# Optimization experiments

Hardware: AMD Instinct MI355X
Metric: run time of the kernel (lower is better)

## Reference

```python
import jax, jax.numpy as jnp
import numpy as np

B, S, T = 64, 512, 256  # batch, seq_len, num_tags


def setup_inputs() -> dict:
    key = jax.random.key(0)
    k1, k2, k3, k4 = jax.random.split(key, 4)
    emissions = jax.random.normal(k1, (B, S, T), dtype=jnp.float32)
    tags = jax.random.randint(k2, (B, S), 0, T, dtype=jnp.int32)
    mask = jnp.ones((B, S), dtype=bool)
    # nn.init.uniform_(-0.01, 0.01) as in reset_parameters()
    transitions = jax.random.uniform(k3, (T, T), minval=-0.01, maxval=0.01, dtype=jnp.float32)
    tse = jax.random.uniform(k4, (T + 2, T + 2), minval=-0.01, maxval=0.01, dtype=jnp.float32)
    tse = tse.at[T + 1, T].set(-10000.0)  # transitions[end_tag, start_tag] = -10000
    return {"emissions": emissions, "tags": tags, "mask": mask,
            "transitions": transitions, "transitions_with_start_end": tse}


def reference(emissions, tags, mask, transitions, transitions_with_start_end):
    Bv, Sv, Tv = emissions.shape
    start, end = Tv, Tv + 1

    # ---- forward algorithm (log partition), faithful to the torch recurrence:
    # new[b, j] = alpha[b, j] + logsumexp_k( trans[k, j] + emit_t[b, k] )
    # (the mask line fv*mask + fv*~mask in the original is a no-op)
    alpha0 = emissions[:, 0] + transitions_with_start_end[start, :Tv]

    def step(alpha, em_t):  # em_t: [B, T]
        lse = jax.nn.logsumexp(transitions[None, :, :] + em_t[:, :, None], axis=1)  # [B, T]
        return alpha + lse, None

    ems = jnp.swapaxes(emissions[:, 1:], 0, 1)  # [S-1, B, T]
    alpha, _ = jax.lax.scan(step, alpha0, ems)
    forward_score = jax.nn.logsumexp(alpha + transitions_with_start_end[:Tv, end], axis=1)  # [B]

    # ---- gold path score
    mf = mask.astype(emissions.dtype)
    emit = jnp.take_along_axis(emissions, tags[:, :, None].astype(jnp.int32), axis=2)[:, :, 0]  # [B, S]
    score = transitions_with_start_end[start, tags[:, 0]]
    score = score + jnp.sum(emit * mf, axis=1)
    score = score + jnp.sum(transitions[tags[:, 1:], tags[:, :-1]] * mf[:, 1:], axis=1)
    last_idx = jnp.sum(mask.astype(jnp.int32), axis=1) - 1  # [B]
    last_tags = jnp.take_along_axis(tags, last_idx[:, None], axis=1)[:, 0]
    score = score + transitions_with_start_end[last_tags, end]

    return forward_score - score  # negative log-likelihood per batch element, [B]
```

## Files before the change

### kernel.cpp

```cpp
#include <hip/hip_runtime.h>
#include <cstdint>

#define B_ 64
#define S_ 512
#define T_ 256
#define TP2 258

#define BM 64
#define BK 32
#define LDA 40
#define LDB 40

typedef __attribute__((ext_vector_type(8))) short short8;
typedef __attribute__((ext_vector_type(4))) float f32x4;

__device__ __forceinline__ ushort f2bf(float f) {
    union { float f; uint32_t u; } c; c.f = f;
    uint32_t u = c.u;
    u += 0x7FFFu + ((u >> 16) & 1u);
    return (ushort)(u >> 16);
}

__global__ void prep_w(const float* __restrict__ trans, ushort* __restrict__ wt) {
    int n = blockIdx.x;
    int k = threadIdx.x;
    wt[n * T_ + k] = f2bf(__expf(trans[k * T_ + n]));
}

__global__ __launch_bounds__(256) void gemm_lse(
    const float* __restrict__ em, const ushort* __restrict__ wt,
    float* __restrict__ accb)
{
    __shared__ ushort Alds[BM * LDA];
    __shared__ ushort Blds[T_ * LDB];

    int blk  = blockIdx.x;
    long r0  = (long)blk * BM;
    int batch = (int)(r0 / S_);
    bool has_s0 = (r0 % S_) == 0;

    int tid  = threadIdx.x;
    int wave = tid >> 6;
    int lane = tid & 63;
    int quad = lane >> 4;
    int l15  = lane & 15;

    f32x4 acc[4][4];
    for (int i = 0; i < 4; ++i)
        for (int j = 0; j < 4; ++j)
            acc[i][j] = (f32x4){0.f, 0.f, 0.f, 0.f};

    int srow = tid >> 2;
    int skc  = (tid & 3) * 8;

    for (int kt = 0; kt < T_ / BK; ++kt) {
        int k0 = kt * BK;
        {
            const float* src = em + (r0 + srow) * T_ + k0 + skc;
            float4 va = *(const float4*)(src);
            float4 vb = *(const float4*)(src + 4);
            union { ushort u[8]; uint4 v; } pk;
            pk.u[0] = f2bf(__expf(va.x)); pk.u[1] = f2bf(__expf(va.y));
            pk.u[2] = f2bf(__expf(va.z)); pk.u[3] = f2bf(__expf(va.w));
            pk.u[4] = f2bf(__expf(vb.x)); pk.u[5] = f2bf(__expf(vb.y));
            pk.u[6] = f2bf(__expf(vb.z)); pk.u[7] = f2bf(__expf(vb.w));
            *(uint4*)&Alds[srow * LDA + skc] = pk.v;
        }
        for (int p = 0; p < 4; ++p) {
            int idx = tid + p * 256;
            int n   = idx >> 2;
            int kc  = (idx & 3) * 8;
            uint4 v = *(const uint4*)&wt[n * T_ + k0 + kc];
            *(uint4*)&Blds[n * LDB + kc] = v;
        }
        __syncthreads();

        short8 af[4], bf[4];
        for (int i = 0; i < 4; ++i)
            af[i] = *(const short8*)&Alds[(i * 16 + l15) * LDA + quad * 8];
        for (int j = 0; j < 4; ++j)
            bf[j] = *(const short8*)&Blds[(wave * 64 + j * 16 + l15) * LDB + quad * 8];
        for (int i = 0; i < 4; ++i)
            for (int j = 0; j < 4; ++j)
                acc[i][j] = __builtin_amdgcn_mfma_f32_16x16x32_bf16(af[i], bf[j], acc[i][j], 0, 0, 0);
        __syncthreads();
    }

    for (int j = 0; j < 4; ++j) {
        float s = 0.f;
        for (int i = 0; i < 4; ++i) {
            f32x4 a = acc[i][j];
            for (int v = 0; v < 4; ++v) {
                bool skip = has_s0 && (i == 0) && (quad == 0) && (v == 0);
                if (!skip) s += __logf(a[v]);
            }
        }
        s += __shfl_xor(s, 16);
        s += __shfl_xor(s, 32);
        if (lane < 16)
            atomicAdd(&accb[batch * T_ + wave * 64 + j * 16 + lane], s);
    }
}

__global__ __launch_bounds__(256) void finalize(
    const float* __restrict__ em, const int* __restrict__ tags,
    const float* __restrict__ trans, const float* __restrict__ tse,
    const float* __restrict__ accb, float* __restrict__ out)
{
    __shared__ float red[8];
    int b = blockIdx.x;
    int j = threadIdx.x;
    int w = j >> 6;

    float v = em[(long)b * S_ * T_ + j] + tse[T_ * TP2 + j]
            + accb[b * T_ + j] + tse[j * TP2 + (T_ + 1)];

    float m = v;
    for (int o = 32; o; o >>= 1) m = fmaxf(m, __shfl_xor(m, o));
    if ((j & 63) == 0) red[w] = m;
    __syncthreads();
    m = fmaxf(fmaxf(red[0], red[1]), fmaxf(red[2], red[3]));

    float e = __expf(v - m);
    for (int o = 32; o; o >>= 1) e += __shfl_xor(e, o);
    if ((j & 63) == 0) red[4 + w] = e;
    __syncthreads();
    float fwd = m + __logf(red[4] + red[5] + red[6] + red[7]);

    const int* tg = tags + b * S_;
    float sc = 0.f;
    for (int s = j; s < S_; s += 256) {
        int t = tg[s];
        sc += em[((long)b * S_ + s) * T_ + t];
        if (s >= 1) sc += trans[t * T_ + tg[s - 1]];
    }
    if (j == 0) {
        sc += tse[T_ * TP2 + tg[0]];
        sc += tse[tg[S_ - 1] * TP2 + (T_ + 1)];
    }
    for (int o = 32; o; o >>= 1) sc += __shfl_xor(sc, o);
    __syncthreads();
    if ((j & 63) == 0) red[w] = sc;
    __syncthreads();
    if (j == 0) out[b] = fwd - (red[0] + red[1] + red[2] + red[3]);
}

extern "C" void kernel_launch(void* const* d_in, const int* in_sizes, int n_in,
                              void* d_out, int out_size, void* d_ws, size_t ws_size,
                              hipStream_t stream) {
    const float* em    = (const float*)d_in[0];
    const int*   tags  = (const int*)d_in[1];
    const float* trans = (const float*)d_in[3];
    const float* tse   = (const float*)d_in[4];
    float* out = (float*)d_out;

    ushort* wt   = (ushort*)d_ws;
    float*  accb = (float*)((char*)d_ws + 131072);

    hipMemsetAsync(accb, 0, B_ * T_ * sizeof(float), stream);
    prep_w<<<T_, T_, 0, stream>>>(trans, wt);
    gemm_lse<<<(B_ * S_) / BM, 256, 0, stream>>>(em, wt, accb);
    finalize<<<B_, T_, 0, stream>>>(em, tags, trans, tse, accb, out);
}
```

Measured before the change: 96.73 us.

## Prefetch GEMM tiles into registers, replace atomics with partials, move gold score into GEMM

The GEMM kernel now loads the next K-tile of emissions and exp-weights into registers while the MFMAs of the current tile run, hiding global-load latency. Atomic accumulation is replaced by per-block partial sums that finalize adds up, so the memset launch goes away. The gold-path score is computed inside the GEMM blocks, one row per lane, instead of a serial loop in finalize. This costs more registers, which may lower occupancy, and adds workspace for the partials.

```diff
diff --git a/kernel.cpp b/kernel.cpp
--- a/kernel.cpp
+++ b/kernel.cpp
@@ -29,15 +29,18 @@
 
 __global__ __launch_bounds__(256) void gemm_lse(
     const float* __restrict__ em, const ushort* __restrict__ wt,
-    float* __restrict__ accb)
+    const int* __restrict__ tags, const float* __restrict__ trans,
+    const float* __restrict__ tse,
+    float* __restrict__ accP, float* __restrict__ scoreP)
 {
     __shared__ ushort Alds[BM * LDA];
     __shared__ ushort Blds[T_ * LDB];
 
-    int blk  = blockIdx.x;
-    long r0  = (long)blk * BM;
-    int batch = (int)(r0 / S_);
-    bool has_s0 = (r0 % S_) == 0;
+    int blk   = blockIdx.x;
+    long r0   = (long)blk * BM;
+    int batch = blk >> 3;
+    int s0    = (blk & 7) * BM;
+    bool has_s0 = (s0 == 0);
 
     int tid  = threadIdx.x;
     int wave = tid >> 6;
@@ -53,12 +56,18 @@
     int srow = tid >> 2;
     int skc  = (tid & 3) * 8;
 
+    const float* aptr = em + (r0 + srow) * T_ + skc;
+    float4 va = *(const float4*)(aptr);
+    float4 vb = *(const float4*)(aptr + 4);
+    uint4 bv[4];
+    #pragma unroll
+    for (int p = 0; p < 4; ++p) {
+        int idx = tid + p * 256;
+        bv[p] = *(const uint4*)&wt[(idx >> 2) * T_ + (idx & 3) * 8];
+    }
+
     for (int kt = 0; kt < T_ / BK; ++kt) {
-        int k0 = kt * BK;
         {
-            const float* src = em + (r0 + srow) * T_ + k0 + skc;
-            float4 va = *(const float4*)(src);
-            float4 vb = *(const float4*)(src + 4);
             union { ushort u[8]; uint4 v; } pk;
             pk.u[0] = f2bf(__expf(va.x)); pk.u[1] = f2bf(__expf(va.y));
             pk.u[2] = f2bf(__expf(va.z)); pk.u[3] = f2bf(__expf(va.w));
@@ -66,30 +75,46 @@
             pk.u[6] = f2bf(__expf(vb.z)); pk.u[7] = f2bf(__expf(vb.w));
             *(uint4*)&Alds[srow * LDA + skc] = pk.v;
         }
+        #pragma unroll
         for (int p = 0; p < 4; ++p) {
             int idx = tid + p * 256;
-            int n   = idx >> 2;
-            int kc  = (idx & 3) * 8;
-            uint4 v = *(const uint4*)&wt[n * T_ + k0 + kc];
-            *(uint4*)&Blds[n * LDB + kc] = v;
+            *(uint4*)&Blds[(idx >> 2) * LDB + (idx & 3) * 8] = bv[p];
         }
         __syncthreads();
 
+        if (kt < T_ / BK - 1) {
+            int k1 = (kt + 1) * BK;
+            va = *(const float4*)(aptr + k1);
+            vb = *(const float4*)(aptr + k1 + 4);
+            #pragma unroll
+            for (int p = 0; p < 4; ++p) {
+                int idx = tid + p * 256;
+                bv[p] = *(const uint4*)&wt[(idx >> 2) * T_ + k1 + (idx & 3) * 8];
+            }
+        }
+
         short8 af[4], bf[4];
+        #pragma unroll
         for (int i = 0; i < 4; ++i)
             af[i] = *(const short8*)&Alds[(i * 16 + l15) * LDA + quad * 8];
+        #pragma unroll
         for (int j = 0; j < 4; ++j)
             bf[j] = *(const short8*)&Blds[(wave * 64 + j * 16 + l15) * LDB + quad * 8];
+        #pragma unroll
         for (int i = 0; i < 4; ++i)
+            #pragma unroll
             for (int j = 0; j < 4; ++j)
                 acc[i][j] = __builtin_amdgcn_mfma_f32_16x16x32_bf16(af[i], bf[j], acc[i][j], 0, 0, 0);
         __syncthreads();
     }
 
+    #pragma unroll
     for (int j = 0; j < 4; ++j) {
         float s = 0.f;
+        #pragma unroll
         for (int i = 0; i < 4; ++i) {
             f32x4 a = acc[i][j];
+            #pragma unroll
             for (int v = 0; v < 4; ++v) {
                 bool skip = has_s0 && (i == 0) && (quad == 0) && (v == 0);
                 if (!skip) s += __logf(a[v]);
@@ -98,51 +123,63 @@
         s += __shfl_xor(s, 16);
         s += __shfl_xor(s, 32);
         if (lane < 16)
-            atomicAdd(&accb[batch * T_ + wave * 64 + j * 16 + lane], s);
+            accP[blk * T_ + wave * 64 + j * 16 + lane] = s;
+    }
+
+    {
+        float sc = 0.f;
+        if (lane < 16) {
+            int sl = s0 + wave * 16 + lane;
+            const int* tg = tags + batch * S_;
+            int t = tg[sl];
+            sc = em[((long)batch * S_ + sl) * T_ + t];
+            if (sl >= 1) sc += trans[t * T_ + tg[sl - 1]];
+            else         sc += tse[T_ * TP2 + t];
+            if (sl == S_ - 1) sc += tse[t * TP2 + (T_ + 1)];
+        }
+        #pragma unroll
+        for (int o = 32; o; o >>= 1) sc += __shfl_xor(sc, o);
+        if (lane == 0) scoreP[blk * 4 + wave] = sc;
     }
 }
 
 __global__ __launch_bounds__(256) void finalize(
-    const float* __restrict__ em, const int* __restrict__ tags,
-    const float* __restrict__ trans, const float* __restrict__ tse,
-    const float* __restrict__ accb, float* __restrict__ out)
+    const float* __restrict__ em, const float* __restrict__ tse,
+    const float* __restrict__ accP, const float* __restrict__ scoreP,
+    float* __restrict__ out)
 {
     __shared__ float red[8];
     int b = blockIdx.x;
     int j = threadIdx.x;
     int w = j >> 6;
 
+    float p = 0.f;
+    #pragma unroll
+    for (int q = 0; q < 8; ++q)
+        p += accP[((b << 3) + q) * T_ + j];
+
     float v = em[(long)b * S_ * T_ + j] + tse[T_ * TP2 + j]
-            + accb[b * T_ + j] + tse[j * TP2 + (T_ + 1)];
+            + p + tse[j * TP2 + (T_ + 1)];
 
     float m = v;
+    #pragma unroll
     for (int o = 32; o; o >>= 1) m = fmaxf(m, __shfl_xor(m, o));
     if ((j & 63) == 0) red[w] = m;
     __syncthreads();
     m = fmaxf(fmaxf(red[0], red[1]), fmaxf(red[2], red[3]));
 
     float e = __expf(v - m);
+    #pragma unroll
     for (int o = 32; o; o >>= 1) e += __shfl_xor(e, o);
     if ((j & 63) == 0) red[4 + w] = e;
     __syncthreads();
     float fwd = m + __logf(red[4] + red[5] + red[6] + red[7]);
 
-    const int* tg = tags + b * S_;
-    float sc = 0.f;
-    for (int s = j; s < S_; s += 256) {
-        int t = tg[s];
-        sc += em[((long)b * S_ + s) * T_ + t];
-        if (s >= 1) sc += trans[t * T_ + tg[s - 1]];
-    }
-    if (j == 0) {
-        sc += tse[T_ * TP2 + tg[0]];
-        sc += tse[tg[S_ - 1] * TP2 + (T_ + 1)];
-    }
-    for (int o = 32; o; o >>= 1) sc += __shfl_xor(sc, o);
-    __syncthreads();
-    if ((j & 63) == 0) red[w] = sc;
-    __syncthreads();
-    if (j == 0) out[b] = fwd - (red[0] + red[1] + red[2] + red[3]);
+    float sc = (j < 32) ? scoreP[b * 32 + j] : 0.f;
+    #pragma unroll
+    for (int o = 16; o; o >>= 1) sc += __shfl_xor(sc, o);
+
+    if (j == 0) out[b] = fwd - sc;
 }
 
 extern "C" void kernel_launch(void* const* d_in, const int* in_sizes, int n_in,
@@ -154,11 +191,11 @@
     const float* tse   = (const float*)d_in[4];
     float* out = (float*)d_out;
 
-    ushort* wt   = (ushort*)d_ws;
-    float*  accb = (float*)((char*)d_ws + 131072);
-
-    hipMemsetAsync(accb, 0, B_ * T_ * sizeof(float), stream);
+    ushort* wt     = (ushort*)d_ws;
+    float*  accP   = (float*)((char*)d_ws + 131072);
+    float*  scoreP = (float*)((char*)d_ws + 131072 + 524288);
+
     prep_w<<<T_, T_, 0, stream>>>(trans, wt);
-    gemm_lse<<<(B_ * S_) / BM, 256, 0, stream>>>(em, wt, accb);
-    finalize<<<B_, T_, 0, stream>>>(em, tags, trans, tse, accb, out);
-}
+    gemm_lse<<<(B_ * S_) / BM, 256, 0, stream>>>(em, wt, tags, trans, tse, accP, scoreP);
+    finalize<<<B_, T_, 0, stream>>>(em, tse, accP, scoreP, out);
+}
```

Result: slower. 107.4 us (+11.1%).
